# Kernel tuning notes

Hardware: AMD Instinct MI355X
Metric: run time of the kernel (lower is better)

The kernel has to match this reference:

```python
import jax, jax.numpy as jnp
import numpy as np

H = 8          # num_heads
DH = 128       # head_dim
NH = 2         # num_householder
HID = 2048     # hidden_size
CONV = 4       # conv kernel size
EPS = 1e-5
KEY_DIM = H * DH


def setup_inputs() -> dict:
    key = jax.random.key(0)
    ks = jax.random.split(key, 16)
    B, L = 2, 1024
    s = 0.02
    return {
        "x": jax.random.normal(ks[0], (B, L, HID), jnp.float32),
        "Wq": jax.random.normal(ks[1], (KEY_DIM, HID), jnp.float32) * s,
        "Wk": jax.random.normal(ks[2], (KEY_DIM * NH, HID), jnp.float32) * s,
        "Wv": jax.random.normal(ks[3], (KEY_DIM * NH, HID), jnp.float32) * s,
        "Wb": jax.random.normal(ks[4], (H * NH, HID), jnp.float32) * s,
        "Wa": jax.random.normal(ks[5], (H, HID), jnp.float32) * s,
        "Wg": jax.random.normal(ks[6], (KEY_DIM, HID), jnp.float32) * s,
        "Wo": jax.random.normal(ks[7], (HID, KEY_DIM), jnp.float32) * s,
        "A_log": jnp.log(jax.random.uniform(ks[8], (H,), jnp.float32, 1.0, 8.0)),
        "dt_bias": jax.random.normal(ks[9], (H,), jnp.float32) * 0.1,
        "conv_q": jax.random.normal(ks[10], (KEY_DIM, CONV), jnp.float32) * 0.3,
        "conv_k": jax.random.normal(ks[11], (KEY_DIM * NH, CONV), jnp.float32) * 0.3,
        "conv_v": jax.random.normal(ks[12], (KEY_DIM * NH, CONV), jnp.float32) * 0.3,
        "o_norm_w": jnp.ones((DH,), jnp.float32),
    }


def _dwconv_silu(x, w):
    # x: (B, L, C); w: (C, K). Depthwise causal conv1d (left pad K-1) + SiLU.
    y = jax.lax.conv_general_dilated(
        x.transpose(0, 2, 1), w[:, None, :], (1,),
        [(w.shape[-1] - 1, 0)], feature_group_count=w.shape[0])
    return jax.nn.silu(y).transpose(0, 2, 1)


def _l2norm(x):
    return x / jnp.maximum(jnp.linalg.norm(x, axis=-1, keepdims=True), 1e-12)


def _forward(x, Wq, Wk, Wv, Wb, Wa, Wg, Wo, A_log, dt_bias,
             conv_q, conv_k, conv_v, o_norm_w):
    B, L, _ = x.shape
    T = L * NH
    # projections + causal depthwise conv + SiLU
    q = _dwconv_silu(x @ Wq.T, conv_q).reshape(B, L, H, DH)
    k = _dwconv_silu(x @ Wk.T, conv_k).reshape(B, T, H, DH)
    v = _dwconv_silu(x @ Wv.T, conv_v).reshape(B, T, H, DH)
    beta = jax.nn.sigmoid(x @ Wb.T).reshape(B, T, H) * 2.0  # allow_neg_eigval
    g = -jnp.exp(A_log) * jax.nn.softplus(x @ Wa.T + dt_bias)  # (B, L, H)
    q = _l2norm(q) / (DH ** 0.5)
    k = _l2norm(k)
    # gate applied only at first householder step; query only at last
    g_full = jnp.zeros((B, L, NH, H), x.dtype).at[:, :, 0].set(g).reshape(B, T, H)
    q_full = jnp.zeros((B, L, NH, H, DH), x.dtype).at[:, :, -1].set(q).reshape(B, T, H, DH)

    def step(state, inp):
        q_t, k_t, v_t, g_t, b_t = inp
        state = state * jnp.exp(g_t)[..., None, None]            # (B,H,K,V)
        corr = jnp.einsum('bhk,bhkv->bhv', k_t, state)
        v_new = (v_t - corr) * b_t[..., None]
        state = state + jnp.einsum('bhk,bhv->bhkv', k_t, v_new)
        o_t = jnp.einsum('bhk,bhkv->bhv', q_t, state)
        return state, o_t

    xs = (q_full.transpose(1, 0, 2, 3), k.transpose(1, 0, 2, 3),
          v.transpose(1, 0, 2, 3), g_full.transpose(1, 0, 2),
          beta.transpose(1, 0, 2))
    state0 = jnp.zeros((B, H, DH, DH), x.dtype)
    final_state, o = jax.lax.scan(step, state0, xs)
    # keep output of last householder sub-step per token
    o = o.transpose(1, 0, 2, 3).reshape(B, L, NH, H, DH)[:, :, -1]  # (B,L,H,DH)
    # gated RMSNorm: rmsnorm(o) * weight * silu(gate)
    gg = (x @ Wg.T).reshape(B, L, H, DH)
    o = o * jax.lax.rsqrt(jnp.mean(o * o, -1, keepdims=True) + EPS)
    o = o * o_norm_w * jax.nn.silu(gg)
    return o.reshape(B, L, KEY_DIM) @ Wo.T, final_state


def reference(x, Wq, Wk, Wv, Wb, Wa, Wg, Wo, A_log, dt_bias,
              conv_q, conv_k, conv_v, o_norm_w):
    return _forward(x, Wq, Wk, Wv, Wb, Wa, Wg, Wo, A_log, dt_bias,
                    conv_q, conv_k, conv_v, o_norm_w)
```

## Files before the change

### kernel.cpp

```cpp
#include <hip/hip_runtime.h>
#include <math.h>

#define B_   2
#define L_   1024
#define H_   8
#define DH_  128
#define NH_  2
#define HID_ 2048
#define T_   (L_ * NH_)
#define KEY_ (H_ * DH_)

typedef __attribute__((ext_vector_type(8))) short short8;
typedef __attribute__((ext_vector_type(4))) float f32x4;
typedef __attribute__((ext_vector_type(2))) float f32x2;

__device__ __forceinline__ ushort f2bf(float f) {
  unsigned u = __float_as_uint(f);
  u += 0x7fffu + ((u >> 16) & 1u);
  return (ushort)(u >> 16);
}

__global__ __launch_bounds__(256) void cvt_bf16(const float* __restrict__ in,
                                                ushort* __restrict__ out, int n4) {
  int i = blockIdx.x * 256 + threadIdx.x;
  if (i >= n4) return;
  float4 v = ((const float4*)in)[i];
  ushort4 o;
  o.x = f2bf(v.x); o.y = f2bf(v.y); o.z = f2bf(v.z); o.w = f2bf(v.w);
  ((ushort4*)out)[i] = o;
}

__device__ __forceinline__ void gload16(const void* g, void* l) {
  __builtin_amdgcn_global_load_lds(
      (const __attribute__((address_space(1))) unsigned*)g,
      (__attribute__((address_space(3))) unsigned*)l, 16, 0, 0);
}

__global__ __launch_bounds__(256) void gemm_bf16(
    const ushort* __restrict__ A, const ushort* __restrict__ W,
    float* __restrict__ C, int M, int N, int K) {
  __shared__ __align__(16) ushort As[128 * 32];
  __shared__ __align__(16) ushort Bs[128 * 32];
  const int tid = threadIdx.x;
  const int lane = tid & 63, wid = tid >> 6;
  const int wr = wid >> 1, wc = wid & 1;
  const int bm = blockIdx.y * 128, bn = blockIdx.x * 128;
  const int srow = tid >> 2, sch = (tid & 3) * 8;
  const ushort* ga = A + (size_t)(bm + srow) * K + sch;
  const ushort* gb = W + (size_t)(bn + srow) * K + sch;
  ushort* la = As + tid * 8;
  ushort* lb = Bs + tid * 8;
  const int frow = lane & 15;
  const int fk = (lane >> 4) * 8;
  f32x4 acc[4][4];
#pragma unroll
  for (int i = 0; i < 4; ++i)
#pragma unroll
    for (int j = 0; j < 4; ++j) acc[i][j] = (f32x4){0.f, 0.f, 0.f, 0.f};

  for (int k0 = 0; k0 < K; k0 += 32) {
    gload16(ga + k0, la);
    gload16(ga + k0 + (size_t)64 * K, la + 64 * 32);
    gload16(gb + k0, lb);
    gload16(gb + k0 + (size_t)64 * K, lb + 64 * 32);
    __syncthreads();
    short8 a[4], b[4];
#pragma unroll
    for (int m = 0; m < 4; ++m)
      a[m] = *(const short8*)(As + (wr * 64 + m * 16 + frow) * 32 + fk);
#pragma unroll
    for (int n = 0; n < 4; ++n)
      b[n] = *(const short8*)(Bs + (wc * 64 + n * 16 + frow) * 32 + fk);
#pragma unroll
    for (int m = 0; m < 4; ++m)
#pragma unroll
      for (int n = 0; n < 4; ++n)
        acc[m][n] = __builtin_amdgcn_mfma_f32_16x16x32_bf16(a[m], b[n], acc[m][n], 0, 0, 0);
    __syncthreads();
  }
  const int crow0 = (lane >> 4) * 4, ccol = lane & 15;
#pragma unroll
  for (int m = 0; m < 4; ++m)
#pragma unroll
    for (int n = 0; n < 4; ++n) {
      float* cp = C + (size_t)(bm + wr * 64 + m * 16 + crow0) * N + bn + wc * 64 + n * 16 + ccol;
#pragma unroll
      for (int j = 0; j < 4; ++j) cp[(size_t)j * N] = acc[m][n][j];
    }
}

template <int MODE>
__global__ __launch_bounds__(256) void gemm_small(
    const float* __restrict__ X, const float* __restrict__ W,
    float* __restrict__ C, int M, int N, int K,
    const float* __restrict__ A_log, const float* __restrict__ dt_bias) {
  const int wid = blockIdx.x * 4 + (threadIdx.x >> 6);
  const int lane = threadIdx.x & 63;
  const int m = wid / N, n = wid - m * N;
  const float* xr = X + (size_t)m * K;
  const float* wr = W + (size_t)n * K;
  float s = 0.f;
  for (int k = lane * 4; k < K; k += 256) {
    const float4 a = *(const float4*)(xr + k);
    const float4 b = *(const float4*)(wr + k);
    s = fmaf(a.x, b.x, s); s = fmaf(a.y, b.y, s);
    s = fmaf(a.z, b.z, s); s = fmaf(a.w, b.w, s);
  }
#pragma unroll
  for (int mm = 32; mm; mm >>= 1) s += __shfl_xor(s, mm);
  if (lane == 0) {
    float r;
    if (MODE == 1) {
      r = 2.f / (1.f + expf(-s));
    } else if (MODE == 2) {
      const float xs = s + dt_bias[n];
      const float sp = (xs > 20.f) ? xs : log1pf(expf(xs));
      r = expf(-expf(A_log[n]) * sp);
    } else {
      r = s;
    }
    C[(size_t)m * N + n] = r;
  }
}

template <int NORM>
__global__ __launch_bounds__(128) void conv_silu_norm(
    const float* __restrict__ in, const float* __restrict__ cw,
    float* __restrict__ out, int C, float scale) {
  const int bl = blockIdx.x;
  const int l = bl & (L_ - 1);
  const int c = blockIdx.y * 128 + threadIdx.x;
  const size_t base = (size_t)bl * C + c;
  const float w0 = cw[c * 4 + 0], w1 = cw[c * 4 + 1];
  const float w2 = cw[c * 4 + 2], w3 = cw[c * 4 + 3];
  float acc = w3 * in[base];
  if (l >= 1) acc = fmaf(w2, in[base - (size_t)C], acc);
  if (l >= 2) acc = fmaf(w1, in[base - 2 * (size_t)C], acc);
  if (l >= 3) acc = fmaf(w0, in[base - 3 * (size_t)C], acc);
  float y = acc / (1.f + expf(-acc));
  if (NORM) {
    float ss = y * y;
#pragma unroll
    for (int mm = 32; mm; mm >>= 1) ss += __shfl_xor(ss, mm);
    __shared__ float p[2];
    if ((threadIdx.x & 63) == 0) p[threadIdx.x >> 6] = ss;
    __syncthreads();
    const float tot = p[0] + p[1];
    y *= scale / fmaxf(sqrtf(tot), 1e-12f);
  }
  out[base] = y;
}


__device__ __forceinline__ float dpp_red8(float x) {
  int t;
  t = __builtin_amdgcn_mov_dpp(__float_as_int(x), 0xB1, 0xf, 0xf, true);
  x += __int_as_float(t);
  t = __builtin_amdgcn_mov_dpp(__float_as_int(x), 0x4E, 0xf, 0xf, true);
  x += __int_as_float(t);
  t = __builtin_amdgcn_mov_dpp(__float_as_int(x), 0x141, 0xf, 0xf, true);
  x += __int_as_float(t);
  return x;
}

union V16 {
  float4 v4[4];
  f32x2  v2[8];
};

struct Tok {
  V16 k0, k1, q;
  float v0, v1, dk, b0, b1;
};

__device__ __forceinline__ void load_tok(Tok& t, int l,
    const float* __restrict__ kp, const float* __restrict__ vp,
    const float* __restrict__ qp, const float* __restrict__ dkp,
    const float* __restrict__ bap) {
  const float* kpt = kp + (size_t)(2 * l) * 1024;
#pragma unroll
  for (int c = 0; c < 4; ++c) t.k0.v4[c] = *(const float4*)(kpt + c * 4);
#pragma unroll
  for (int c = 0; c < 4; ++c) t.k1.v4[c] = *(const float4*)(kpt + 1024 + c * 4);
  t.v0 = vp[(size_t)(2 * l) * 1024];
  t.v1 = vp[(size_t)(2 * l) * 1024 + 1024];
  const float* qpt = qp + (size_t)l * 1024;
#pragma unroll
  for (int c = 0; c < 4; ++c) t.q.v4[c] = *(const float4*)(qpt + c * 4);
  t.dk = dkp[l * 8];
  t.b0 = bap[l * 16];
  t.b1 = bap[l * 16 + 8];
}

__device__ __forceinline__ void proc_tok(const Tok& t, int l,
                                         f32x2 st[8], int kg, float* __restrict__ op) {
  const f32x2 d2 = {t.dk, t.dk};
  f32x2 a0 = {0.f, 0.f}, a1 = a0, a2 = a0, a3 = a0;
#pragma unroll
  for (int p = 0; p < 8; p += 4) {
    st[p + 0] *= d2;
    st[p + 1] *= d2;
    st[p + 2] *= d2;
    st[p + 3] *= d2;
    a0 = __builtin_elementwise_fma(t.k0.v2[p + 0], st[p + 0], a0);
    a1 = __builtin_elementwise_fma(t.k0.v2[p + 1], st[p + 1], a1);
    a2 = __builtin_elementwise_fma(t.k0.v2[p + 2], st[p + 2], a2);
    a3 = __builtin_elementwise_fma(t.k0.v2[p + 3], st[p + 3], a3);
  }
  f32x2 sp2 = (a0 + a1) + (a2 + a3);
  float corr = dpp_red8(sp2.x + sp2.y);
  const float vn0 = (t.v0 - corr) * t.b0;
  const f32x2 w0 = {vn0, vn0};
#pragma unroll
  for (int p = 0; p < 8; ++p)
    st[p] = __builtin_elementwise_fma(t.k0.v2[p], w0, st[p]);

  a0 = (f32x2){0.f, 0.f}; a1 = a0; a2 = a0; a3 = a0;
#pragma unroll
  for (int p = 0; p < 8; p += 4) {
    a0 = __builtin_elementwise_fma(t.k1.v2[p + 0], st[p + 0], a0);
    a1 = __builtin_elementwise_fma(t.k1.v2[p + 1], st[p + 1], a1);
    a2 = __builtin_elementwise_fma(t.k1.v2[p + 2], st[p + 2], a2);
    a3 = __builtin_elementwise_fma(t.k1.v2[p + 3], st[p + 3], a3);
  }
  sp2 = (a0 + a1) + (a2 + a3);
  corr = dpp_red8(sp2.x + sp2.y);
  const float vn1 = (t.v1 - corr) * t.b1;
  const f32x2 w1 = {vn1, vn1};
  a0 = (f32x2){0.f, 0.f}; a1 = a0; a2 = a0; a3 = a0;
#pragma unroll
  for (int p = 0; p < 8; p += 4) {
    st[p + 0] = __builtin_elementwise_fma(t.k1.v2[p + 0], w1, st[p + 0]);
    st[p + 1] = __builtin_elementwise_fma(t.k1.v2[p + 1], w1, st[p + 1]);
    st[p + 2] = __builtin_elementwise_fma(t.k1.v2[p + 2], w1, st[p + 2]);
    st[p + 3] = __builtin_elementwise_fma(t.k1.v2[p + 3], w1, st[p + 3]);
    a0 = __builtin_elementwise_fma(t.q.v2[p + 0], st[p + 0], a0);
    a1 = __builtin_elementwise_fma(t.q.v2[p + 1], st[p + 1], a1);
    a2 = __builtin_elementwise_fma(t.q.v2[p + 2], st[p + 2], a2);
    a3 = __builtin_elementwise_fma(t.q.v2[p + 3], st[p + 3], a3);
  }
  sp2 = (a0 + a1) + (a2 + a3);
  const float osum = dpp_red8(sp2.x + sp2.y);
  if (kg == 0) op[(size_t)l * 1024] = osum;
}

__global__ __launch_bounds__(64, 1) void scan_kernel(
    const float* __restrict__ qn, const float* __restrict__ kn,
    const float* __restrict__ vc, const float* __restrict__ ba,
    const float* __restrict__ dka, float* __restrict__ o,
    float* __restrict__ fstate) {
  const int bid = blockIdx.x;
  const int xcd = bid & 7;
  const int rest = bid >> 3;
  const int vb = rest & 15;
  const int g = ((rest >> 4) << 3) + xcd;
  const int h = g & 7;
  const int b = g >> 3;
  const int lane = threadIdx.x;
  const int kg = lane & 7, vl = lane >> 3;
  const int v = vb * 8 + vl;
  const float* kp = kn + (size_t)b * T_ * 1024 + h * 128 + kg * 16;
  const float* vp = vc + (size_t)b * T_ * 1024 + h * 128 + v;
  const float* qp = qn + (size_t)b * L_ * 1024 + h * 128 + kg * 16;
  const float* dkp = dka + (size_t)b * L_ * 8 + h;
  const float* bap = ba + (size_t)b * L_ * 16 + h;
  float* op = o + (size_t)b * L_ * 1024 + h * 128 + v;

  f32x2 st[8];
#pragma unroll
  for (int j = 0; j < 8; ++j) st[j] = (f32x2){0.f, 0.f};

  Tok t0, t1, t2, t3;
  load_tok(t0, 0, kp, vp, qp, dkp, bap);
  load_tok(t1, 1, kp, vp, qp, dkp, bap);
  load_tok(t2, 2, kp, vp, qp, dkp, bap);
  load_tok(t3, 3, kp, vp, qp, dkp, bap);
  for (int l = 0; l < L_; l += 4) {
    proc_tok(t0, l, st, kg, op);
    if (l + 4 < L_) load_tok(t0, l + 4, kp, vp, qp, dkp, bap);
    proc_tok(t1, l + 1, st, kg, op);
    if (l + 5 < L_) load_tok(t1, l + 5, kp, vp, qp, dkp, bap);
    proc_tok(t2, l + 2, st, kg, op);
    if (l + 6 < L_) load_tok(t2, l + 6, kp, vp, qp, dkp, bap);
    proc_tok(t3, l + 3, st, kg, op);
    if (l + 7 < L_) load_tok(t3, l + 7, kp, vp, qp, dkp, bap);
  }
  float* fp = fstate + (size_t)(b * H_ + h) * (128 * 128) + (size_t)(kg * 16) * 128 + v;
#pragma unroll
  for (int p = 0; p < 8; ++p) {
    fp[(size_t)(2 * p) * 128] = st[p].x;
    fp[(size_t)(2 * p + 1) * 128] = st[p].y;
  }
}

__global__ __launch_bounds__(128) void rmsnorm_gate(
    const float* __restrict__ o, const float* __restrict__ gg,
    const float* __restrict__ w, ushort* __restrict__ on) {
  const int blk = blockIdx.x;
  const int d = threadIdx.x;
  const size_t base = (size_t)blk * 128 + d;
  const float x = o[base];
  float ss = x * x;
#pragma unroll
  for (int mm = 32; mm; mm >>= 1) ss += __shfl_xor(ss, mm);
  __shared__ float p[2];
  if ((d & 63) == 0) p[d >> 6] = ss;
  __syncthreads();
  const float tot = p[0] + p[1];
  const float r = rsqrtf(tot * (1.f / 128.f) + 1e-5f);
  const float gv = gg[base];
  on[base] = f2bf(x * r * w[d] * (gv / (1.f + expf(-gv))));
}

extern "C" void kernel_launch(void* const* d_in, const int* in_sizes, int n_in,
                              void* d_out, int out_size, void* d_ws, size_t ws_size,
                              hipStream_t stream) {
  const float* x       = (const float*)d_in[0];
  const float* Wq      = (const float*)d_in[1];
  const float* Wk      = (const float*)d_in[2];
  const float* Wv      = (const float*)d_in[3];
  const float* Wb      = (const float*)d_in[4];
  const float* Wa      = (const float*)d_in[5];
  const float* Wg      = (const float*)d_in[6];
  const float* Wo      = (const float*)d_in[7];
  const float* A_log   = (const float*)d_in[8];
  const float* dt_bias = (const float*)d_in[9];
  const float* conv_q  = (const float*)d_in[10];
  const float* conv_k  = (const float*)d_in[11];
  const float* conv_v  = (const float*)d_in[12];
  const float* o_norm_w= (const float*)d_in[13];

  float* ws = (float*)d_ws;
  float* pa = ws;
  float* kn = pa + 4194304;
  float* vc = kn + 4194304;
  float* qn = vc + 4194304;
  float* gg = qn + 2097152;
  float* ba = gg + 2097152;
  float* dka = ba + 32768;
  ushort* xb  = (ushort*)(dka + 16384);
  ushort* wb  = xb + 4194304;
  ushort* pab = wb + 4194304;

  float* out = (float*)d_out;
  float* fstate = out + (size_t)B_ * L_ * HID_;

  const int M = B_ * L_;

  cvt_bf16<<<4096, 256, 0, stream>>>(x, xb, 1048576);
  cvt_bf16<<<4096, 256, 0, stream>>>(Wk, wb, 1048576);
  gemm_bf16<<<dim3(16, 16), 256, 0, stream>>>(xb, wb, pa, M, 2048, HID_);
  conv_silu_norm<1><<<dim3(M, 16), 128, 0, stream>>>(pa, conv_k, kn, 2048, 1.0f);
  cvt_bf16<<<4096, 256, 0, stream>>>(Wv, wb, 1048576);
  gemm_bf16<<<dim3(16, 16), 256, 0, stream>>>(xb, wb, pa, M, 2048, HID_);
  conv_silu_norm<0><<<dim3(M, 16), 128, 0, stream>>>(pa, conv_v, vc, 2048, 1.0f);
  cvt_bf16<<<2048, 256, 0, stream>>>(Wq, wb, 524288);
  gemm_bf16<<<dim3(8, 16), 256, 0, stream>>>(xb, wb, pa, M, KEY_, HID_);
  conv_silu_norm<1><<<dim3(M, 8), 128, 0, stream>>>(pa, conv_q, qn, KEY_,
                                                    0.08838834764831845f);
  cvt_bf16<<<2048, 256, 0, stream>>>(Wg, wb, 524288);
  gemm_bf16<<<dim3(8, 16), 256, 0, stream>>>(xb, wb, gg, M, KEY_, HID_);
  gemm_small<1><<<dim3(M * 16 / 4), 256, 0, stream>>>(x, Wb, ba, M, 16, HID_, nullptr, nullptr);
  gemm_small<2><<<dim3(M * 8 / 4), 256, 0, stream>>>(x, Wa, dka, M, 8, HID_, A_log, dt_bias);
  scan_kernel<<<dim3(B_ * H_ * 16), 64, 0, stream>>>(qn, kn, vc, ba, dka, pa, fstate);
  rmsnorm_gate<<<dim3(M * H_), 128, 0, stream>>>(pa, gg, o_norm_w, pab);
  cvt_bf16<<<2048, 256, 0, stream>>>(Wo, wb, 524288);
  gemm_bf16<<<dim3(16, 16), 256, 0, stream>>>(pab, wb, out, M, HID_, KEY_);
}
```

Baseline: 888.1 us.

## Precompute per-token key/query dot products so scan does one fused state pass

Adds a dots_kernel that precomputes k0·k1, q·k0 and q·k1 per token along with the decay and beta scalars. The scan then takes all three reductions against the old state in parallel and derives the corrections algebraically, instead of chaining three dependent reduce-and-update passes. Each token now needs one state update pass instead of several. The scan also doubles its block count (16 k-lanes per v column, 4 state pairs per lane) to shorten each lane's work and raise parallelism. The cost is an extra small kernel and workspace buffer, plus slightly different floating-point rounding order.

```diff
diff --git a/kernel.cpp b/kernel.cpp
--- a/kernel.cpp
+++ b/kernel.cpp
@@ -151,8 +151,39 @@
   out[base] = y;
 }
 
-
-__device__ __forceinline__ float dpp_red8(float x) {
+__global__ __launch_bounds__(256) void dots_kernel(
+    const float* __restrict__ kn, const float* __restrict__ qn,
+    const float* __restrict__ dka, const float* __restrict__ ba,
+    float* __restrict__ sc) {
+  const int idx = blockIdx.x * 4 + (threadIdx.x >> 6);
+  const int lane = threadIdx.x & 63;
+  const int h = idx & 7;
+  const int bl = idx >> 3;
+  const int l = bl & (L_ - 1);
+  const int b = bl >> 10;
+  const float* k0 = kn + ((size_t)b * T_ + 2 * l) * 1024 + h * 128;
+  const float* k1 = k0 + 1024;
+  const float* q  = qn + (size_t)bl * 1024 + h * 128;
+  const f32x2 k0v = *(const f32x2*)(k0 + lane * 2);
+  const f32x2 k1v = *(const f32x2*)(k1 + lane * 2);
+  const f32x2 qv  = *(const f32x2*)(q + lane * 2);
+  const f32x2 p00 = k1v * k0v, pq0 = qv * k0v, pq1 = qv * k1v;
+  float d00 = p00.x + p00.y, dq0 = pq0.x + pq0.y, dq1 = pq1.x + pq1.y;
+#pragma unroll
+  for (int mm = 32; mm; mm >>= 1) {
+    d00 += __shfl_xor(d00, mm);
+    dq0 += __shfl_xor(dq0, mm);
+    dq1 += __shfl_xor(dq1, mm);
+  }
+  if (lane == 0) {
+    float4* dst = (float4*)(sc + (size_t)idx * 8);
+    dst[0] = (float4){dka[bl * 8 + h], ba[bl * 16 + h], ba[bl * 16 + 8 + h], d00};
+    dst[1] = (float4){dq0, dq1, 0.f, 0.f};
+  }
+}
+
+
+__device__ __forceinline__ float dpp_red16(float x) {
   int t;
   t = __builtin_amdgcn_mov_dpp(__float_as_int(x), 0xB1, 0xf, 0xf, true);
   x += __int_as_float(t);
@@ -160,134 +191,110 @@
   x += __int_as_float(t);
   t = __builtin_amdgcn_mov_dpp(__float_as_int(x), 0x141, 0xf, 0xf, true);
   x += __int_as_float(t);
+  t = __builtin_amdgcn_mov_dpp(__float_as_int(x), 0x140, 0xf, 0xf, true);
+  x += __int_as_float(t);
   return x;
 }
 
-union V16 {
-  float4 v4[4];
-  f32x2  v2[8];
+union V8 {
+  float4 v4[2];
+  f32x2  v2[4];
 };
 
 struct Tok {
-  V16 k0, k1, q;
-  float v0, v1, dk, b0, b1;
+  V8 k0, k1, q;
+  float4 s0, s1;
+  float v0, v1;
 };
 
 __device__ __forceinline__ void load_tok(Tok& t, int l,
     const float* __restrict__ kp, const float* __restrict__ vp,
-    const float* __restrict__ qp, const float* __restrict__ dkp,
-    const float* __restrict__ bap) {
+    const float* __restrict__ qp, const float* __restrict__ scp) {
   const float* kpt = kp + (size_t)(2 * l) * 1024;
-#pragma unroll
-  for (int c = 0; c < 4; ++c) t.k0.v4[c] = *(const float4*)(kpt + c * 4);
-#pragma unroll
-  for (int c = 0; c < 4; ++c) t.k1.v4[c] = *(const float4*)(kpt + 1024 + c * 4);
+  t.k0.v4[0] = *(const float4*)(kpt);
+  t.k0.v4[1] = *(const float4*)(kpt + 4);
+  t.k1.v4[0] = *(const float4*)(kpt + 1024);
+  t.k1.v4[1] = *(const float4*)(kpt + 1028);
+  const float* qpt = qp + (size_t)l * 1024;
+  t.q.v4[0] = *(const float4*)(qpt);
+  t.q.v4[1] = *(const float4*)(qpt + 4);
+  const float* scl = scp + (size_t)l * 64;
+  t.s0 = *(const float4*)(scl);
+  t.s1 = *(const float4*)(scl + 4);
   t.v0 = vp[(size_t)(2 * l) * 1024];
   t.v1 = vp[(size_t)(2 * l) * 1024 + 1024];
-  const float* qpt = qp + (size_t)l * 1024;
-#pragma unroll
-  for (int c = 0; c < 4; ++c) t.q.v4[c] = *(const float4*)(qpt + c * 4);
-  t.dk = dkp[l * 8];
-  t.b0 = bap[l * 16];
-  t.b1 = bap[l * 16 + 8];
 }
 
 __device__ __forceinline__ void proc_tok(const Tok& t, int l,
-                                         f32x2 st[8], int kg, float* __restrict__ op) {
-  const f32x2 d2 = {t.dk, t.dk};
-  f32x2 a0 = {0.f, 0.f}, a1 = a0, a2 = a0, a3 = a0;
-#pragma unroll
-  for (int p = 0; p < 8; p += 4) {
-    st[p + 0] *= d2;
-    st[p + 1] *= d2;
-    st[p + 2] *= d2;
-    st[p + 3] *= d2;
-    a0 = __builtin_elementwise_fma(t.k0.v2[p + 0], st[p + 0], a0);
-    a1 = __builtin_elementwise_fma(t.k0.v2[p + 1], st[p + 1], a1);
-    a2 = __builtin_elementwise_fma(t.k0.v2[p + 2], st[p + 2], a2);
-    a3 = __builtin_elementwise_fma(t.k0.v2[p + 3], st[p + 3], a3);
-  }
-  f32x2 sp2 = (a0 + a1) + (a2 + a3);
-  float corr = dpp_red8(sp2.x + sp2.y);
-  const float vn0 = (t.v0 - corr) * t.b0;
-  const f32x2 w0 = {vn0, vn0};
-#pragma unroll
-  for (int p = 0; p < 8; ++p)
-    st[p] = __builtin_elementwise_fma(t.k0.v2[p], w0, st[p]);
-
-  a0 = (f32x2){0.f, 0.f}; a1 = a0; a2 = a0; a3 = a0;
-#pragma unroll
-  for (int p = 0; p < 8; p += 4) {
-    a0 = __builtin_elementwise_fma(t.k1.v2[p + 0], st[p + 0], a0);
-    a1 = __builtin_elementwise_fma(t.k1.v2[p + 1], st[p + 1], a1);
-    a2 = __builtin_elementwise_fma(t.k1.v2[p + 2], st[p + 2], a2);
-    a3 = __builtin_elementwise_fma(t.k1.v2[p + 3], st[p + 3], a3);
-  }
-  sp2 = (a0 + a1) + (a2 + a3);
-  corr = dpp_red8(sp2.x + sp2.y);
-  const float vn1 = (t.v1 - corr) * t.b1;
-  const f32x2 w1 = {vn1, vn1};
-  a0 = (f32x2){0.f, 0.f}; a1 = a0; a2 = a0; a3 = a0;
-#pragma unroll
-  for (int p = 0; p < 8; p += 4) {
-    st[p + 0] = __builtin_elementwise_fma(t.k1.v2[p + 0], w1, st[p + 0]);
-    st[p + 1] = __builtin_elementwise_fma(t.k1.v2[p + 1], w1, st[p + 1]);
-    st[p + 2] = __builtin_elementwise_fma(t.k1.v2[p + 2], w1, st[p + 2]);
-    st[p + 3] = __builtin_elementwise_fma(t.k1.v2[p + 3], w1, st[p + 3]);
-    a0 = __builtin_elementwise_fma(t.q.v2[p + 0], st[p + 0], a0);
-    a1 = __builtin_elementwise_fma(t.q.v2[p + 1], st[p + 1], a1);
-    a2 = __builtin_elementwise_fma(t.q.v2[p + 2], st[p + 2], a2);
-    a3 = __builtin_elementwise_fma(t.q.v2[p + 3], st[p + 3], a3);
-  }
-  sp2 = (a0 + a1) + (a2 + a3);
-  const float osum = dpp_red8(sp2.x + sp2.y);
-  if (kg == 0) op[(size_t)l * 1024] = osum;
+                                         f32x2 st[4], int lane, float* __restrict__ op) {
+  f32x2 a0, a1, b0v, b1v, c0v, c1v;
+  a0  = t.k0.v2[0] * st[0]; a0  = __builtin_elementwise_fma(t.k0.v2[2], st[2], a0);
+  a1  = t.k0.v2[1] * st[1]; a1  = __builtin_elementwise_fma(t.k0.v2[3], st[3], a1);
+  b0v = t.k1.v2[0] * st[0]; b0v = __builtin_elementwise_fma(t.k1.v2[2], st[2], b0v);
+  b1v = t.k1.v2[1] * st[1]; b1v = __builtin_elementwise_fma(t.k1.v2[3], st[3], b1v);
+  c0v = t.q.v2[0]  * st[0]; c0v = __builtin_elementwise_fma(t.q.v2[2],  st[2], c0v);
+  c1v = t.q.v2[1]  * st[1]; c1v = __builtin_elementwise_fma(t.q.v2[3],  st[3], c1v);
+  const f32x2 sa = a0 + a1, sb = b0v + b1v, sq = c0v + c1v;
+  const float c0 = dpp_red16(sa.x + sa.y);
+  const float c1 = dpp_red16(sb.x + sb.y);
+  const float cq = dpp_red16(sq.x + sq.y);
+  const float g = t.s0.x, bb0 = t.s0.y, bb1 = t.s0.z, d00 = t.s0.w;
+  const float dq0 = t.s1.x, dq1 = t.s1.y;
+  const float vn0 = (t.v0 - g * c0) * bb0;
+  const float vn1 = (t.v1 - fmaf(d00, vn0, g * c1)) * bb1;
+  const float osum = fmaf(dq1, vn1, fmaf(dq0, vn0, g * cq));
+  const f32x2 g2 = {g, g}, w0 = {vn0, vn0}, w1 = {vn1, vn1};
+#pragma unroll
+  for (int p = 0; p < 4; ++p) {
+    f32x2 s = st[p] * g2;
+    s = __builtin_elementwise_fma(t.k0.v2[p], w0, s);
+    st[p] = __builtin_elementwise_fma(t.k1.v2[p], w1, s);
+  }
+  if ((lane & 15) == 0) op[(size_t)l * 1024] = osum;
 }
 
 __global__ __launch_bounds__(64, 1) void scan_kernel(
     const float* __restrict__ qn, const float* __restrict__ kn,
-    const float* __restrict__ vc, const float* __restrict__ ba,
-    const float* __restrict__ dka, float* __restrict__ o,
-    float* __restrict__ fstate) {
+    const float* __restrict__ vc, const float* __restrict__ sc,
+    float* __restrict__ o, float* __restrict__ fstate) {
   const int bid = blockIdx.x;
   const int xcd = bid & 7;
   const int rest = bid >> 3;
-  const int vb = rest & 15;
-  const int g = ((rest >> 4) << 3) + xcd;
+  const int vb = rest & 31;
+  const int g = ((rest >> 5) << 3) + xcd;
   const int h = g & 7;
   const int b = g >> 3;
   const int lane = threadIdx.x;
-  const int kg = lane & 7, vl = lane >> 3;
-  const int v = vb * 8 + vl;
-  const float* kp = kn + (size_t)b * T_ * 1024 + h * 128 + kg * 16;
+  const int kg = lane & 15, vl = lane >> 4;
+  const int v = vb * 4 + vl;
+  const float* kp = kn + (size_t)b * T_ * 1024 + h * 128 + kg * 8;
   const float* vp = vc + (size_t)b * T_ * 1024 + h * 128 + v;
-  const float* qp = qn + (size_t)b * L_ * 1024 + h * 128 + kg * 16;
-  const float* dkp = dka + (size_t)b * L_ * 8 + h;
-  const float* bap = ba + (size_t)b * L_ * 16 + h;
+  const float* qp = qn + (size_t)b * L_ * 1024 + h * 128 + kg * 8;
+  const float* scp = sc + ((size_t)b * L_ * 8 + h) * 8;
   float* op = o + (size_t)b * L_ * 1024 + h * 128 + v;
 
-  f32x2 st[8];
-#pragma unroll
-  for (int j = 0; j < 8; ++j) st[j] = (f32x2){0.f, 0.f};
+  f32x2 st[4];
+#pragma unroll
+  for (int j = 0; j < 4; ++j) st[j] = (f32x2){0.f, 0.f};
 
   Tok t0, t1, t2, t3;
-  load_tok(t0, 0, kp, vp, qp, dkp, bap);
-  load_tok(t1, 1, kp, vp, qp, dkp, bap);
-  load_tok(t2, 2, kp, vp, qp, dkp, bap);
-  load_tok(t3, 3, kp, vp, qp, dkp, bap);
+  load_tok(t0, 0, kp, vp, qp, scp);
+  load_tok(t1, 1, kp, vp, qp, scp);
+  load_tok(t2, 2, kp, vp, qp, scp);
+  load_tok(t3, 3, kp, vp, qp, scp);
   for (int l = 0; l < L_; l += 4) {
-    proc_tok(t0, l, st, kg, op);
-    if (l + 4 < L_) load_tok(t0, l + 4, kp, vp, qp, dkp, bap);
-    proc_tok(t1, l + 1, st, kg, op);
-    if (l + 5 < L_) load_tok(t1, l + 5, kp, vp, qp, dkp, bap);
-    proc_tok(t2, l + 2, st, kg, op);
-    if (l + 6 < L_) load_tok(t2, l + 6, kp, vp, qp, dkp, bap);
-    proc_tok(t3, l + 3, st, kg, op);
-    if (l + 7 < L_) load_tok(t3, l + 7, kp, vp, qp, dkp, bap);
-  }
-  float* fp = fstate + (size_t)(b * H_ + h) * (128 * 128) + (size_t)(kg * 16) * 128 + v;
-#pragma unroll
-  for (int p = 0; p < 8; ++p) {
+    proc_tok(t0, l, st, lane, op);
+    if (l + 4 < L_) load_tok(t0, l + 4, kp, vp, qp, scp);
+    proc_tok(t1, l + 1, st, lane, op);
+    if (l + 5 < L_) load_tok(t1, l + 5, kp, vp, qp, scp);
+    proc_tok(t2, l + 2, st, lane, op);
+    if (l + 6 < L_) load_tok(t2, l + 6, kp, vp, qp, scp);
+    proc_tok(t3, l + 3, st, lane, op);
+    if (l + 7 < L_) load_tok(t3, l + 7, kp, vp, qp, scp);
+  }
+  float* fp = fstate + (size_t)(b * H_ + h) * (128 * 128) + (size_t)(kg * 8) * 128 + v;
+#pragma unroll
+  for (int p = 0; p < 4; ++p) {
     fp[(size_t)(2 * p) * 128] = st[p].x;
     fp[(size_t)(2 * p + 1) * 128] = st[p].y;
   }
@@ -341,6 +348,7 @@
   ushort* xb  = (ushort*)(dka + 16384);
   ushort* wb  = xb + 4194304;
   ushort* pab = wb + 4194304;
+  float* sc = (float*)(pab + 2097152);
 
   float* out = (float*)d_out;
   float* fstate = out + (size_t)B_ * L_ * HID_;
@@ -362,7 +370,8 @@
   gemm_bf16<<<dim3(8, 16), 256, 0, stream>>>(xb, wb, gg, M, KEY_, HID_);
   gemm_small<1><<<dim3(M * 16 / 4), 256, 0, stream>>>(x, Wb, ba, M, 16, HID_, nullptr, nullptr);
   gemm_small<2><<<dim3(M * 8 / 4), 256, 0, stream>>>(x, Wa, dka, M, 8, HID_, A_log, dt_bias);
-  scan_kernel<<<dim3(B_ * H_ * 16), 64, 0, stream>>>(qn, kn, vc, ba, dka, pa, fstate);
+  dots_kernel<<<dim3(M * H_ / 4), 256, 0, stream>>>(kn, qn, dka, ba, sc);
+  scan_kernel<<<dim3(B_ * H_ * 32), 64, 0, stream>>>(qn, kn, vc, sc, pa, fstate);
   rmsnorm_gate<<<dim3(M * H_), 128, 0, stream>>>(pa, gg, o_norm_w, pab);
   cvt_bf16<<<2048, 256, 0, stream>>>(Wo, wb, 524288);
   gemm_bf16<<<dim3(16, 16), 256, 0, stream>>>(pab, wb, out, M, HID_, KEY_);
```

After: 901.0 us. Within noise of the previous version (+1.5%).
